# Optimization experiments

Measured on AMD Instinct MI355X. Metric: run time of the kernel, lower is better.

## Reference

```python
import jax, jax.numpy as jnp
import numpy as np

VOCAB, EMBED, HIDDEN = 512, 512, 1024
BATCH, SEQ = 128, 1024


def setup_inputs() -> dict:
    key = jax.random.key(0)
    ks = jax.random.split(key, 9)
    inp = {
        "input_ids": jax.random.randint(ks[0], (BATCH, SEQ), 0, VOCAB),
        "embedding": jax.random.normal(ks[1], (VOCAB, EMBED), dtype=jnp.float32),
        "w_xh0": jax.random.normal(ks[2], (HIDDEN, EMBED), dtype=jnp.float32) * 0.05,
        "w_hh0": jax.random.normal(ks[3], (HIDDEN, HIDDEN), dtype=jnp.float32) * 0.05,
        "b_h0": jnp.zeros((HIDDEN,), dtype=jnp.float32),
        "w_xh1": jax.random.normal(ks[4], (HIDDEN, HIDDEN), dtype=jnp.float32) * 0.05,
        "w_hh1": jax.random.normal(ks[5], (HIDDEN, HIDDEN), dtype=jnp.float32) * 0.05,
        "b_h1": jnp.zeros((HIDDEN,), dtype=jnp.float32),
        "w_hy": jax.random.normal(ks[6], (VOCAB, HIDDEN), dtype=jnp.float32) * 0.05,
        "b_y": jnp.zeros((VOCAB,), dtype=jnp.float32),
    }
    return inp


def reference(input_ids, embedding, w_xh0, w_hh0, b_h0, w_xh1, w_hh1, b_h1, w_hy, b_y):
    # dropout_prob = 0.0 -> dropouts are identity (eval-mode math)
    emb = embedding[input_ids]                # [B, T, E]
    emb_t = jnp.swapaxes(emb, 0, 1)           # [T, B, E] for scan over time
    B = input_ids.shape[0]
    h0_init = jnp.zeros((B, HIDDEN), dtype=embedding.dtype)
    h1_init = jnp.zeros((B, HIDDEN), dtype=embedding.dtype)

    def step(carry, x_t):
        h0, h1 = carry
        h0 = jnp.tanh(x_t @ w_xh0.T + h0 @ w_hh0.T + b_h0)
        h1 = jnp.tanh(h0 @ w_xh1.T + h1 @ w_hh1.T + b_h1)
        logits_t = h1 @ w_hy.T + b_y           # [B, V]
        return (h0, h1), logits_t

    (h0, h1), logits_t = jax.lax.scan(step, (h0_init, h1_init), emb_t)
    logits = jnp.swapaxes(logits_t, 0, 1)      # [B, T, V]
    return logits, h0, h1
```

## Files before the change

### kernel.cpp

```cpp
#include <hip/hip_runtime.h>

#define SEQ_T 1024
#define HID   1024
#define EMB   512
#define VOC   512

typedef _Float16 f16;
typedef _Float16 half8 __attribute__((ext_vector_type(8)));
typedef float floatx4 __attribute__((ext_vector_type(4)));

__device__ __forceinline__ float tanh_fast(float x) {
  float e = __expf(2.0f * x);
  return 1.0f - 2.0f / (e + 1.0f);
}

__device__ __forceinline__ half8 ld_cc(const f16* p) {
  half8 v;
  asm volatile("global_load_dwordx4 %0, %1, off sc0 sc1"
               : "=v"(v) : "v"(p) : "memory");
  return v;
}
__device__ __forceinline__ void st_cc(f16* p, f16 x) {
  unsigned v = (unsigned)__builtin_bit_cast(unsigned short, x);
  asm volatile("global_store_short %0, %1, off sc0 sc1"
               :: "v"(p), "v"(v) : "memory");
}
__device__ __forceinline__ void st_flag(unsigned* p, unsigned v) {
  asm volatile("global_store_dword %0, %1, off sc0 sc1"
               :: "v"(p), "v"(v) : "memory");
}
#define VMCNT(n) asm volatile("s_waitcnt vmcnt(" #n ")" ::: "memory")

__device__ __forceinline__ void spin_flags(const unsigned* pA, const unsigned* pB,
                                           unsigned ta, unsigned tb) {
  for (;;) {
    unsigned a, b;
    asm volatile("global_load_dword %0, %2, off sc0 sc1\n\t"
                 "global_load_dword %1, %3, off sc0 sc1\n\t"
                 "s_waitcnt vmcnt(0)"
                 : "=&v"(a), "=&v"(b) : "v"(pA), "v"(pB) : "memory");
    if (__ballot((a >= ta) && (b >= tb)) == ~0ull) return;
    __builtin_amdgcn_s_sleep(1);
  }
}

__global__ void cvt_f32_f16(const float* __restrict__ src, f16* __restrict__ dst, int n) {
  int i = blockIdx.x * 256 + threadIdx.x;
  if (i < n) dst[i] = (f16)src[i];
}

__global__ __launch_bounds__(256) void phaseA(
    const int* __restrict__ ids, const f16* __restrict__ embh,
    const f16* __restrict__ wxh0h, const float* __restrict__ bh0,
    f16* __restrict__ X0)
{
  int bx = blockIdx.x;
  int mt = bx >> 4, nt = bx & 15;
  int wave = threadIdx.x >> 6, lane = threadIdx.x & 63;
  int m0 = mt * 64 + (wave & 1) * 32;
  int n0 = nt * 64 + (wave >> 1) * 32;
  int l15 = lane & 15, q = lane >> 4;

  int mA = m0 + l15, mB = mA + 16;
  const f16* a0p = embh + (size_t)ids[(mA & 127) * SEQ_T + (mA >> 7)] * EMB + q * 8;
  const f16* a1p = embh + (size_t)ids[(mB & 127) * SEQ_T + (mB >> 7)] * EMB + q * 8;
  const f16* b0p = wxh0h + (size_t)(n0 + l15) * EMB + q * 8;
  const f16* b1p = wxh0h + (size_t)(n0 + 16 + l15) * EMB + q * 8;

  floatx4 acc[2][2] = {};
  for (int k = 0; k < EMB; k += 32) {
    half8 a0 = *(const half8*)(a0p + k);
    half8 a1 = *(const half8*)(a1p + k);
    half8 b0 = *(const half8*)(b0p + k);
    half8 b1 = *(const half8*)(b1p + k);
    acc[0][0] = __builtin_amdgcn_mfma_f32_16x16x32_f16(a0, b0, acc[0][0], 0, 0, 0);
    acc[0][1] = __builtin_amdgcn_mfma_f32_16x16x32_f16(a0, b1, acc[0][1], 0, 0, 0);
    acc[1][0] = __builtin_amdgcn_mfma_f32_16x16x32_f16(a1, b0, acc[1][0], 0, 0, 0);
    acc[1][1] = __builtin_amdgcn_mfma_f32_16x16x32_f16(a1, b1, acc[1][1], 0, 0, 0);
  }
  for (int i = 0; i < 2; i++)
    for (int j = 0; j < 2; j++) {
      int col = n0 + j * 16 + l15;
      float bias = bh0[col];
      for (int e = 0; e < 4; e++) {
        int row = m0 + i * 16 + q * 4 + e;
        X0[(size_t)row * HID + col] = (f16)(acc[i][j][e] + bias);
      }
    }
}

__global__ __launch_bounds__(256, 1) void rnn_persist(
    const float* __restrict__ whh0, const float* __restrict__ wxh1,
    const float* __restrict__ whh1, const float* __restrict__ bh1,
    const f16* __restrict__ X0, f16* __restrict__ h0buf, f16* __restrict__ h1buf,
    f16* __restrict__ H1, unsigned* __restrict__ flags)
{
  __shared__ half8 lds[4096];

  const int wg = blockIdx.x;
  const int r = wg >> 4;
  const int c = wg & 15;
  const int wave = threadIdx.x >> 6;
  const int lane = threadIdx.x & 63;
  const int l15 = lane & 15, q = lane >> 4;
  const int r0 = r * 16;
  const int col = c * 64 + wave * 16 + l15;

  unsigned* fA = flags + r * 1024;
  unsigned* fB = flags + 8192 + r * 1024;
  unsigned* myA = fA + (c * 4 + wave) * 16;
  unsigned* myB = fB + (c * 4 + wave) * 16;
  const unsigned* pollA = fA + lane * 16;
  const unsigned* pollB = fB + lane * 16;

  half8 wa[32], wbx[32], wbh[32];
  {
    const float* w0 = whh0 + (size_t)col * HID + q * 8;
    const float* w1 = wxh1 + (size_t)col * HID + q * 8;
    const float* w2 = whh1 + (size_t)col * HID + q * 8;
    #pragma unroll
    for (int i = 0; i < 32; i++) {
      const float* p0 = w0 + i * 32;
      const float* p1 = w1 + i * 32;
      const float* p2 = w2 + i * 32;
      #pragma unroll
      for (int j = 0; j < 8; j++) {
        wa[i][j]  = (f16)p0[j];
        wbx[i][j] = (f16)p1[j];
        wbh[i][j] = (f16)p2[j];
      }
    }
  }
  const float bias1 = bh1[col];

  for (int t = 0; t <= SEQ_T; t++) {
    const f16* h0prev  = h0buf + (size_t)(t & 1) * 131072;
    f16*       h0next  = h0buf + (size_t)((t + 1) & 1) * 131072;
    const f16* h1prev2 = h1buf + (size_t)((t + 1) & 1) * 131072;
    f16*       h1new   = h1buf + (size_t)(t & 1) * 131072;

    f16 xv[4];
    if (t < SEQ_T) {
      const f16* x0t = X0 + (size_t)t * 131072;
      #pragma unroll
      for (int e = 0; e < 4; e++)
        xv[e] = x0t[(size_t)(r0 + q * 4 + e) * HID + col];
    }

    if (t >= 1)
      spin_flags(pollA, pollB, (unsigned)t, (unsigned)(t >= 2 ? t - 1 : 0));

    const f16* ap0 = h0prev  + (size_t)(r0 + l15) * HID + q * 8;
    const f16* ap1 = h1prev2 + (size_t)(r0 + l15) * HID + q * 8;
    half8 v0[8], v1[8];
    #pragma unroll
    for (int i = 0; i < 8; i++) v0[i] = ld_cc(ap0 + (8 * wave + i) * 32);
    #pragma unroll
    for (int i = 0; i < 8; i++) v1[i] = ld_cc(ap1 + (8 * wave + i) * 32);
    VMCNT(8);
    #pragma unroll
    for (int i = 0; i < 8; i++) lds[(8 * wave + i) * 64 + lane] = v0[i];
    VMCNT(0);
    #pragma unroll
    for (int i = 0; i < 8; i++) lds[2048 + (8 * wave + i) * 64 + lane] = v1[i];
    __syncthreads();

    if (t < SEQ_T) {
      floatx4 a0 = {}, a1 = {};
      #pragma unroll
      for (int i = 0; i < 16; i++) {
        half8 f0 = lds[i * 64 + lane];
        half8 f1 = lds[(16 + i) * 64 + lane];
        a0 = __builtin_amdgcn_mfma_f32_16x16x32_f16(f0, wa[i],      a0, 0, 0, 0);
        a1 = __builtin_amdgcn_mfma_f32_16x16x32_f16(f1, wa[16 + i], a1, 0, 0, 0);
      }
      #pragma unroll
      for (int e = 0; e < 4; e++) {
        int row = r0 + q * 4 + e;
        float vv = a0[e] + a1[e] + (float)xv[e];
        st_cc(h0next + (size_t)row * HID + col, (f16)tanh_fast(vv));
      }
    }

    floatx4 b0 = {}, b1 = {};
    if (t >= 1) {
      #pragma unroll
      for (int i = 0; i < 32; i++) {
        half8 f0 = lds[i * 64 + lane];
        half8 f1 = lds[2048 + i * 64 + lane];
        b0 = __builtin_amdgcn_mfma_f32_16x16x32_f16(f0, wbx[i], b0, 0, 0, 0);
        b1 = __builtin_amdgcn_mfma_f32_16x16x32_f16(f1, wbh[i], b1, 0, 0, 0);
      }
    }

    if (t < SEQ_T) {
      VMCNT(0);
      if (lane == 0) st_flag(myA, (unsigned)(t + 1));
    }

    if (t >= 1) {
      f16 hv[4];
      #pragma unroll
      for (int e = 0; e < 4; e++) {
        int row = r0 + q * 4 + e;
        hv[e] = (f16)tanh_fast(b0[e] + b1[e] + bias1);
        st_cc(h1new + (size_t)row * HID + col, hv[e]);
      }
      VMCNT(0);
      if (lane == 0) st_flag(myB, (unsigned)t);
      f16* h1t = H1 + (size_t)(t - 1) * 131072;
      #pragma unroll
      for (int e = 0; e < 4; e++) {
        int row = r0 + q * 4 + e;
        h1t[(size_t)row * HID + col] = hv[e];
      }
    }
    __syncthreads();
  }
}

__global__ __launch_bounds__(256) void logitsK(
    const f16* __restrict__ H1, const f16* __restrict__ whyh,
    const float* __restrict__ by, float* __restrict__ out)
{
  int bx = blockIdx.x;
  int mt = bx >> 3, nt = bx & 7;
  int wave = threadIdx.x >> 6, lane = threadIdx.x & 63;
  int m0 = mt * 64 + (wave & 1) * 32;
  int n0 = nt * 64 + (wave >> 1) * 32;
  int l15 = lane & 15, q = lane >> 4;

  const f16* a0p = H1 + (size_t)(m0 + l15) * HID + q * 8;
  const f16* a1p = H1 + (size_t)(m0 + 16 + l15) * HID + q * 8;
  const f16* b0p = whyh + (size_t)(n0 + l15) * HID + q * 8;
  const f16* b1p = whyh + (size_t)(n0 + 16 + l15) * HID + q * 8;

  floatx4 acc[2][2] = {};
  for (int k = 0; k < HID; k += 32) {
    half8 a0 = *(const half8*)(a0p + k);
    half8 a1 = *(const half8*)(a1p + k);
    half8 b0 = *(const half8*)(b0p + k);
    half8 b1 = *(const half8*)(b1p + k);
    acc[0][0] = __builtin_amdgcn_mfma_f32_16x16x32_f16(a0, b0, acc[0][0], 0, 0, 0);
    acc[0][1] = __builtin_amdgcn_mfma_f32_16x16x32_f16(a0, b1, acc[0][1], 0, 0, 0);
    acc[1][0] = __builtin_amdgcn_mfma_f32_16x16x32_f16(a1, b0, acc[1][0], 0, 0, 0);
    acc[1][1] = __builtin_amdgcn_mfma_f32_16x16x32_f16(a1, b1, acc[1][1], 0, 0, 0);
  }
  for (int i = 0; i < 2; i++)
    for (int j = 0; j < 2; j++) {
      int col = n0 + j * 16 + l15;
      float bias = by[col];
      for (int e = 0; e < 4; e++) {
        int row = m0 + i * 16 + q * 4 + e;
        int t = row >> 7, b = row & 127;
        out[((size_t)b * SEQ_T + t) * VOC + col] = acc[i][j][e] + bias;
      }
    }
}

__global__ void finals(const f16* __restrict__ h0, const f16* __restrict__ h1,
                       float* __restrict__ out) {
  int i = blockIdx.x * 256 + threadIdx.x;
  out[(size_t)67108864 + i] = (float)h0[i];
  out[(size_t)67108864 + 131072 + i] = (float)h1[i];
}

extern "C" void kernel_launch(void* const* d_in, const int* in_sizes, int n_in,
                              void* d_out, int out_size, void* d_ws, size_t ws_size,
                              hipStream_t stream) {
  const int*   ids  = (const int*)d_in[0];
  const float* emb  = (const float*)d_in[1];
  const float* wxh0 = (const float*)d_in[2];
  const float* whh0 = (const float*)d_in[3];
  const float* bh0  = (const float*)d_in[4];
  const float* wxh1 = (const float*)d_in[5];
  const float* whh1 = (const float*)d_in[6];
  const float* bh1  = (const float*)d_in[7];
  const float* why  = (const float*)d_in[8];
  const float* by   = (const float*)d_in[9];
  float* out = (float*)d_out;

  char* ws = (char*)d_ws;
  f16* embh   = (f16*)(ws + 0);
  f16* wxh0h  = (f16*)(ws + 524288);
  f16* whyh   = (f16*)(ws + 1572864);
  f16* h0buf  = (f16*)(ws + 2621440);
  f16* h1buf  = (f16*)(ws + 3145728);
  unsigned* flags = (unsigned*)(ws + 3670016);
  f16* X0     = (f16*)(ws + 4194304);
  f16* H1     = (f16*)(ws + 272629760);

  cvt_f32_f16<<<1024, 256, 0, stream>>>(emb,  embh,  262144);
  cvt_f32_f16<<<2048, 256, 0, stream>>>(wxh0, wxh0h, 524288);
  cvt_f32_f16<<<2048, 256, 0, stream>>>(why,  whyh,  524288);
  hipMemsetAsync(ws + 2621440, 0, 1114112, stream);

  phaseA<<<32768, 256, 0, stream>>>(ids, embh, wxh0h, bh0, X0);

  rnn_persist<<<128, 256, 0, stream>>>(whh0, wxh1, whh1, bh1,
                                       X0, h0buf, h1buf, H1, flags);

  logitsK<<<16384, 256, 0, stream>>>(H1, whyh, by, out);
  finals<<<512, 256, 0, stream>>>(h0buf, h1buf, out);
}
```

Measured before the change: 9.643 ms.

## Use one per-workgroup flag per step and fuse MFMA loops in persistent RNN

Replaces the per-wave dual A/B flags with a single flag per workgroup, written after a block barrier. Each wave now polls only 16 flags with one load instead of 64+64. Hidden-state loads drop the sc1 bit and rely on an agent-scope acquire fence. The h0 and h1 input MFMAs are interleaved in one loop sharing LDS reads. In exchange, h1 and h0 completion are now coupled to one flag. MFMAs also run unconditionally at the boundary steps, and the extra block barrier before the flag store may add latency.

```diff
diff --git a/kernel.cpp b/kernel.cpp
--- a/kernel.cpp
+++ b/kernel.cpp
@@ -14,9 +14,9 @@
   return 1.0f - 2.0f / (e + 1.0f);
 }
 
-__device__ __forceinline__ half8 ld_cc(const f16* p) {
+__device__ __forceinline__ half8 ld_l2(const f16* p) {
   half8 v;
-  asm volatile("global_load_dwordx4 %0, %1, off sc0 sc1"
+  asm volatile("global_load_dwordx4 %0, %1, off sc0"
                : "=v"(v) : "v"(p) : "memory");
   return v;
 }
@@ -31,16 +31,14 @@
 }
 #define VMCNT(n) asm volatile("s_waitcnt vmcnt(" #n ")" ::: "memory")
 
-__device__ __forceinline__ void spin_flags(const unsigned* pA, const unsigned* pB,
-                                           unsigned ta, unsigned tb) {
+__device__ __forceinline__ void spin_row(const unsigned* p, unsigned tgt) {
   for (;;) {
-    unsigned a, b;
-    asm volatile("global_load_dword %0, %2, off sc0 sc1\n\t"
-                 "global_load_dword %1, %3, off sc0 sc1\n\t"
+    unsigned v;
+    asm volatile("global_load_dword %0, %1, off sc0 sc1\n\t"
                  "s_waitcnt vmcnt(0)"
-                 : "=&v"(a), "=&v"(b) : "v"(pA), "v"(pB) : "memory");
-    if (__ballot((a >= ta) && (b >= tb)) == ~0ull) return;
-    __builtin_amdgcn_s_sleep(1);
+                 : "=v"(v) : "v"(p) : "memory");
+    if (__ballot(v >= tgt) == ~0ull) return;
+    __builtin_amdgcn_s_sleep(2);
   }
 }
 
@@ -106,12 +104,8 @@
   const int r0 = r * 16;
   const int col = c * 64 + wave * 16 + l15;
 
-  unsigned* fA = flags + r * 1024;
-  unsigned* fB = flags + 8192 + r * 1024;
-  unsigned* myA = fA + (c * 4 + wave) * 16;
-  unsigned* myB = fB + (c * 4 + wave) * 16;
-  const unsigned* pollA = fA + lane * 16;
-  const unsigned* pollB = fB + lane * 16;
+  unsigned* myflag = flags + r * 256 + c * 16;
+  const unsigned* pollp = flags + r * 256 + (lane & 15) * 16;
 
   half8 wa[32], wbx[32], wbh[32];
   {
@@ -147,16 +141,17 @@
         xv[e] = x0t[(size_t)(r0 + q * 4 + e) * HID + col];
     }
 
-    if (t >= 1)
-      spin_flags(pollA, pollB, (unsigned)t, (unsigned)(t >= 2 ? t - 1 : 0));
+    if (t >= 1) spin_row(pollp, (unsigned)t);
+
+    __builtin_amdgcn_fence(__ATOMIC_ACQUIRE, "agent");
 
     const f16* ap0 = h0prev  + (size_t)(r0 + l15) * HID + q * 8;
     const f16* ap1 = h1prev2 + (size_t)(r0 + l15) * HID + q * 8;
     half8 v0[8], v1[8];
     #pragma unroll
-    for (int i = 0; i < 8; i++) v0[i] = ld_cc(ap0 + (8 * wave + i) * 32);
-    #pragma unroll
-    for (int i = 0; i < 8; i++) v1[i] = ld_cc(ap1 + (8 * wave + i) * 32);
+    for (int i = 0; i < 8; i++) v0[i] = ld_l2(ap0 + (8 * wave + i) * 32);
+    #pragma unroll
+    for (int i = 0; i < 8; i++) v1[i] = ld_l2(ap1 + (8 * wave + i) * 32);
     VMCNT(8);
     #pragma unroll
     for (int i = 0; i < 8; i++) lds[(8 * wave + i) * 64 + lane] = v0[i];
@@ -165,15 +160,18 @@
     for (int i = 0; i < 8; i++) lds[2048 + (8 * wave + i) * 64 + lane] = v1[i];
     __syncthreads();
 
+    floatx4 a0 = {}, a1 = {}, bx0 = {}, bx1 = {};
+    #pragma unroll
+    for (int i = 0; i < 16; i++) {
+      half8 f0 = lds[(2 * i) * 64 + lane];
+      half8 f1 = lds[(2 * i + 1) * 64 + lane];
+      a0  = __builtin_amdgcn_mfma_f32_16x16x32_f16(f0, wa[2 * i],      a0,  0, 0, 0);
+      a1  = __builtin_amdgcn_mfma_f32_16x16x32_f16(f1, wa[2 * i + 1],  a1,  0, 0, 0);
+      bx0 = __builtin_amdgcn_mfma_f32_16x16x32_f16(f0, wbx[2 * i],     bx0, 0, 0, 0);
+      bx1 = __builtin_amdgcn_mfma_f32_16x16x32_f16(f1, wbx[2 * i + 1], bx1, 0, 0, 0);
+    }
+
     if (t < SEQ_T) {
-      floatx4 a0 = {}, a1 = {};
-      #pragma unroll
-      for (int i = 0; i < 16; i++) {
-        half8 f0 = lds[i * 64 + lane];
-        half8 f1 = lds[(16 + i) * 64 + lane];
-        a0 = __builtin_amdgcn_mfma_f32_16x16x32_f16(f0, wa[i],      a0, 0, 0, 0);
-        a1 = __builtin_amdgcn_mfma_f32_16x16x32_f16(f1, wa[16 + i], a1, 0, 0, 0);
-      }
       #pragma unroll
       for (int e = 0; e < 4; e++) {
         int row = r0 + q * 4 + e;
@@ -182,32 +180,30 @@
       }
     }
 
-    floatx4 b0 = {}, b1 = {};
+    floatx4 bh0a = {}, bh1a = {};
+    #pragma unroll
+    for (int i = 0; i < 16; i++) {
+      half8 g0 = lds[2048 + (2 * i) * 64 + lane];
+      half8 g1 = lds[2048 + (2 * i + 1) * 64 + lane];
+      bh0a = __builtin_amdgcn_mfma_f32_16x16x32_f16(g0, wbh[2 * i],     bh0a, 0, 0, 0);
+      bh1a = __builtin_amdgcn_mfma_f32_16x16x32_f16(g1, wbh[2 * i + 1], bh1a, 0, 0, 0);
+    }
+
+    f16 hv[4];
     if (t >= 1) {
       #pragma unroll
-      for (int i = 0; i < 32; i++) {
-        half8 f0 = lds[i * 64 + lane];
-        half8 f1 = lds[2048 + i * 64 + lane];
-        b0 = __builtin_amdgcn_mfma_f32_16x16x32_f16(f0, wbx[i], b0, 0, 0, 0);
-        b1 = __builtin_amdgcn_mfma_f32_16x16x32_f16(f1, wbh[i], b1, 0, 0, 0);
-      }
-    }
-
-    if (t < SEQ_T) {
-      VMCNT(0);
-      if (lane == 0) st_flag(myA, (unsigned)(t + 1));
-    }
+      for (int e = 0; e < 4; e++) {
+        int row = r0 + q * 4 + e;
+        hv[e] = (f16)tanh_fast(bx0[e] + bx1[e] + bh0a[e] + bh1a[e] + bias1);
+        st_cc(h1new + (size_t)row * HID + col, hv[e]);
+      }
+    }
+
+    VMCNT(0);
+    __syncthreads();
+    if (threadIdx.x == 0) st_flag(myflag, (unsigned)(t + 1));
 
     if (t >= 1) {
-      f16 hv[4];
-      #pragma unroll
-      for (int e = 0; e < 4; e++) {
-        int row = r0 + q * 4 + e;
-        hv[e] = (f16)tanh_fast(b0[e] + b1[e] + bias1);
-        st_cc(h1new + (size_t)row * HID + col, hv[e]);
-      }
-      VMCNT(0);
-      if (lane == 0) st_flag(myB, (unsigned)t);
       f16* h1t = H1 + (size_t)(t - 1) * 131072;
       #pragma unroll
       for (int e = 0; e < 4; e++) {
@@ -215,7 +211,6 @@
         h1t[(size_t)row * HID + col] = hv[e];
       }
     }
-    __syncthreads();
   }
 }
 
```

New measurement: 8.144 ms. 1.18x faster.
